# Performance work log

Hardware: AMD Instinct MI355X
Metric: run time of the kernel (lower is better)

## Reference

```python
import jax, jax.numpy as jnp
import numpy as np

# Model dims
T, B, J, H, K, N_LAYERS = 512, 64, 256, 256, 25, 3
THETA = 1.0        # spike threshold
SIGMA_INIT = 0.5   # Dcls gaussian sigma (frozen, requires_grad=False)
EPS = 1e-5         # batchnorm eps
ALPHA = 5.0        # ATan surrogate alpha


@jax.custom_vjp
def atan_spike(v):
    # Heaviside forward, ATan surrogate backward (spikingjelly ATan, alpha=5)
    return (v > 0.0).astype(v.dtype)

def _atan_fwd(v):
    return atan_spike(v), v

def _atan_bwd(v, g):
    return (g * (ALPHA / 2.0) / (1.0 + (jnp.pi / 2.0 * ALPHA * v) ** 2),)

atan_spike.defvjp(_atan_fwd, _atan_bwd)


def gauss_kernel(W, P, sig):
    # Dcls1d version='gauss', kernel_count=1: gaussian-interpolated dense kernel.
    # W, P: (O, Jin) -> kernel (O, Jin, K)
    pos = jnp.arange(K, dtype=W.dtype)                  # dilated kernel positions
    c = P + K // 2                                      # shift P into [0, K)
    s = jnp.abs(sig) + 0.27                             # DCLS sigma floor
    g = jnp.exp(-0.5 * ((pos[None, None, :] - c[..., None]) / s) ** 2)
    g = g / (jnp.sum(g, axis=-1, keepdims=True) + 1e-7)  # normalize over positions
    return W[..., None] * g


def delay_lif_layer(x, W, P, beta, gamma, bb, U0):
    # x: (T, B, Jin) -> (T, B, O)
    kern = gauss_kernel(W, P, SIGMA_INIT)               # (O, Jin, K)
    xc = jnp.transpose(x, (1, 2, 0))                    # (B, Jin, T)
    y = jax.lax.conv_general_dilated(
        xc, kern, window_strides=(1,), padding=[(K - 1, 0)],  # causal left-pad
        dimension_numbers=('NCH', 'OIH', 'NCH'))        # (B, O, T)
    y = jnp.transpose(y, (2, 0, 1))                     # (T, B, O)
    # BatchNorm1d over the flattened (T*B) dim, per channel (training stats)
    mu = jnp.mean(y, axis=(0, 1))
    var = jnp.var(y, axis=(0, 1))
    y = (y - mu) * jax.lax.rsqrt(var + EPS) * gamma + bb

    # Soft-reset LIF recurrence over time (note: original passes RAW beta,
    # not sigmoid(beta), to the cell -- reproduced faithfully here).
    def step(carry, xt):
        Ut, St = carry
        Ut = beta * (Ut - THETA * St) + (1.0 - beta) * xt
        St = atan_spike(Ut - THETA)
        return (Ut, St), St

    _, o = jax.lax.scan(step, (U0, jnp.zeros_like(U0)), y)
    return o


def setup_inputs():
    key = jax.random.key(0)
    ks = jax.random.split(key, 5)
    # sparse binary spike input, [T, B, J]
    x = (jax.random.uniform(ks[0], (T, B, J)) < 0.2).astype(jnp.float32)
    bound = float(np.sqrt(6.0 / J))  # kaiming_uniform, relu gain, fan_in = J*1
    W = jax.random.uniform(ks[1], (N_LAYERS, H, J), minval=-bound, maxval=bound, dtype=jnp.float32)
    P = jax.random.uniform(ks[2], (N_LAYERS, H, J), minval=-(K // 2), maxval=K // 2, dtype=jnp.float32)
    beta = jax.random.uniform(ks[3], (N_LAYERS, H), minval=0.7, maxval=0.9, dtype=jnp.float32)
    gamma = jnp.ones((N_LAYERS, H), jnp.float32)
    bb = jnp.zeros((N_LAYERS, H), jnp.float32)
    U0 = jax.random.uniform(ks[4], (N_LAYERS, B, H), dtype=jnp.float32)  # RandomBatchwiseInit(0,1)
    return {"x": x, "W": W, "P": P, "beta": beta, "gamma": gamma, "bb": bb, "U0": U0}


def reference(x, W, P, beta, gamma, bb, U0):
    o = x
    for l in range(N_LAYERS):  # fixed small layer loop
        o = delay_lif_layer(o, W[l], P[l], beta[l], gamma[l], bb[l], U0[l])
    return o
```

## Files before the change

### kernel.cpp

```cpp
#include <hip/hip_runtime.h>
#include <math.h>

#define T_DIM 512
#define B_DIM 64
#define J_DIM 256
#define H_DIM 256
#define K_TAP 25
#define NL    3
#define M_DIM (T_DIM*B_DIM)
#define NBH   (B_DIM*H_DIM)
#define GUARD_ROWS 1536
#define GUARD_BYTES (GUARD_ROWS*J_DIM)

#define MB 128
#define NB 64
#define NST (K_TAP*(J_DIM/64))
#define BSET 20480

typedef __attribute__((ext_vector_type(4))) int   i32x4;

__device__ __forceinline__ void gl16(const void* g, void* l){
  __builtin_amdgcn_global_load_lds((const __attribute__((address_space(1))) unsigned int*)g,
                                   (__attribute__((address_space(3))) unsigned int*)l, 16, 0, 0);
}

__global__ void zero_guard_k(unsigned char* __restrict__ g, unsigned char* __restrict__ p){
  const int bid = blockIdx.x;
  if(bid < 96) *(uint4*)(g + (size_t)(bid*256 + threadIdx.x)*16) = (uint4){0,0,0,0};
  else         *(uint4*)(p + (size_t)((bid-96)*256 + threadIdx.x)*16) = (uint4){0,0,0,0};
}

__global__ void cast_u8_k(const float* __restrict__ x, unsigned char* __restrict__ s){
  const int i = blockIdx.x*256 + threadIdx.x;
  const float4 v = *(const float4*)(x + (size_t)i*4);
  uchar4 o; o.x=(unsigned char)v.x; o.y=(unsigned char)v.y;
  o.z=(unsigned char)v.z; o.w=(unsigned char)v.w;
  *(uchar4*)(s + (size_t)i*4) = o;
}

__global__ void build_kern_k(const float* __restrict__ W, const float* __restrict__ P,
                             signed char* __restrict__ k0, signed char* __restrict__ k1,
                             signed char* __restrict__ k2, float* __restrict__ fsc, int layer){
  __shared__ float red[256];
  const int o = blockIdx.x, j = threadIdx.x;
  const float w = W[(layer*H_DIM + o)*J_DIM + j];
  const float p = P[(layer*H_DIM + o)*J_DIM + j];
  const float c = p + 12.0f;
  const float sg = 0.77f;
  float v[K_TAP]; float ssum = 0.f;
#pragma unroll
  for(int k=0;k<K_TAP;k++){ float z = ((float)k - c)/sg; v[k] = expf(-0.5f*z*z); ssum += v[k]; }
  const float inv = 1.0f/(ssum + 1e-7f);
  float mv = 0.f;
#pragma unroll
  for(int k=0;k<K_TAP;k++){ v[k] = w * (v[k]*inv); mv = fmaxf(mv, fabsf(v[k])); }
  red[j] = mv; __syncthreads();
  for(int st=128; st; st>>=1){ if(j<st) red[j] = fmaxf(red[j], red[j+st]); __syncthreads(); }
  int e; frexpf(red[0], &e);
  const float invq = ldexpf(1.f, 22 - e);
#pragma unroll
  for(int k=0;k<K_TAP;k++){
    const int d = (K_TAP-1)-k;
    int q = (int)lrintf(v[k]*invq);
    const int b0 = (int)(signed char)(q & 0xFF); q = (q - b0) >> 8;
    const int b1 = (int)(signed char)(q & 0xFF); q = (q - b1) >> 8;
    const size_t idx = (size_t)(d*H_DIM + o)*J_DIM + j;
    k0[idx] = (signed char)b0; k1[idx] = (signed char)b1; k2[idx] = (signed char)q;
  }
  if(j==0) fsc[o] = ldexpf(1.f, e - 22);
}

__global__ __launch_bounds__(256,2) void conv_mfma_k(const unsigned char* __restrict__ spk,
    const signed char* __restrict__ k0, const signed char* __restrict__ k1,
    const signed char* __restrict__ k2, const float* __restrict__ fsc,
    float* __restrict__ y, long long* __restrict__ part){
  __shared__ unsigned char lds[3][BSET];
  const int tid = threadIdx.x, lane = tid & 63, wave = tid >> 6;
  const int bid = blockIdx.x;
  const int q   = (bid & 7)*128 + (bid >> 3);
  const int m0  = (q & 255) * MB;
  const int n0  = (q >> 8) * NB;
  const int wm0 = (wave >> 1) << 6;
  const int wn0 = (wave & 1) << 5;

  const int srow  = tid >> 2;
  const int sslot = ((tid & 3) ^ (srow >> 1)) & 3;
  const int rslot = ((((lane>>4) ^ (lane>>1)) & 3) << 4);

  i32x4 acc0[4][2], acc1[4][2], acc2[4][2];
#pragma unroll
  for(int m=0;m<4;m++)
#pragma unroll
    for(int n=0;n<2;n++){
      acc0[m][n] = (i32x4){0,0,0,0};
      acc1[m][n] = (i32x4){0,0,0,0};
      acc2[m][n] = (i32x4){0,0,0,0};
    }

#define STAGE(base,t) do{ \
    const int d_ = (t)>>2, jc_ = ((t)&3)<<6; \
    unsigned char* lb_ = (base); \
    const unsigned char* as_ = spk + (size_t)(m0 + srow - (d_<<6) + GUARD_ROWS)*J_DIM + jc_ + sslot*16; \
    gl16(as_,                    lb_        + wave*1024); \
    gl16(as_ + (size_t)64*J_DIM, lb_ + 4096 + wave*1024); \
    const size_t bo_ = (size_t)(d_*H_DIM + n0 + srow)*J_DIM + jc_ + sslot*16; \
    gl16(k0 + bo_, lb_ + 8192  + wave*1024); \
    gl16(k1 + bo_, lb_ + 12288 + wave*1024); \
    gl16(k2 + bo_, lb_ + 16384 + wave*1024); \
  }while(0)

  unsigned char* const L = &lds[0][0];

  STAGE(L, 0);
  STAGE(L + BSET, 1);

  int rb = 0;
  for(int t=0; t<NST; ++t){
    if(t < NST-1) asm volatile("s_waitcnt vmcnt(5)" ::: "memory");
    else          asm volatile("s_waitcnt vmcnt(0)" ::: "memory");
    __builtin_amdgcn_s_barrier();
    __builtin_amdgcn_sched_barrier(0);
    unsigned char* Lb = L + rb*BSET;
    i32x4 af[4], b0f[2], b1f[2], b2f[2];
#pragma unroll
    for(int m=0;m<4;m++)
      af[m] = *(const i32x4*)(Lb + (wm0 + m*16 + (lane&15))*64 + rslot);
#pragma unroll
    for(int n=0;n<2;n++){
      const int ro = (wn0 + n*16 + (lane&15))*64 + rslot;
      b0f[n] = *(const i32x4*)(Lb + 8192  + ro);
      b1f[n] = *(const i32x4*)(Lb + 12288 + ro);
      b2f[n] = *(const i32x4*)(Lb + 16384 + ro);
    }
    if(t+2 < NST){
      int sb = rb + 2; if(sb >= 3) sb -= 3;
      STAGE(L + sb*BSET, t+2);
    }
    __builtin_amdgcn_s_setprio(1);
#pragma unroll
    for(int m=0;m<4;m++)
#pragma unroll
      for(int n=0;n<2;n++){
        acc0[m][n] = __builtin_amdgcn_mfma_i32_16x16x64_i8(af[m], b0f[n], acc0[m][n], 0,0,0);
        acc1[m][n] = __builtin_amdgcn_mfma_i32_16x16x64_i8(af[m], b1f[n], acc1[m][n], 0,0,0);
        acc2[m][n] = __builtin_amdgcn_mfma_i32_16x16x64_i8(af[m], b2f[n], acc2[m][n], 0,0,0);
      }
    __builtin_amdgcn_s_setprio(0);
    rb += 1; if(rb == 3) rb = 0;
  }

  const int r0 = m0 + wm0 + ((lane>>4)<<2);
  const int c0 = n0 + wn0 + (lane&15);
  const double f0 = (double)fsc[c0];
  const double f1 = (double)fsc[c0+16];
#pragma unroll
  for(int n=0;n<2;n++){
    const double fs = n ? f1 : f0;
    long long s1 = 0; unsigned long long shi = 0, slo = 0;
#pragma unroll
    for(int m=0;m<4;m++)
#pragma unroll
      for(int r=0;r<4;r++){
        const long long cmb = ((long long)acc2[m][n][r] << 16)
                            + ((long long)acc1[m][n][r] << 8)
                            +  (long long)acc0[m][n][r];
        y[(size_t)(r0 + m*16 + r)*H_DIM + c0 + n*16] = (float)((double)cmb * fs);
        s1 += cmb;
        const __int128 sq = (__int128)cmb * cmb;
        slo += (unsigned long long)(unsigned int)sq;
        shi += (unsigned long long)(sq >> 32);
      }
    s1  += __shfl_xor(s1, 16);  s1  += __shfl_xor(s1, 32);
    shi += __shfl_xor(shi, 16); shi += __shfl_xor(shi, 32);
    slo += __shfl_xor(slo, 16); slo += __shfl_xor(slo, 32);
    if(lane < 16){
      const int c = c0 + n*16;
      atomicAdd((unsigned long long*)&part[c],       (unsigned long long)s1);
      atomicAdd((unsigned long long*)&part[256 + c], shi);
      atomicAdd((unsigned long long*)&part[512 + c], slo);
    }
  }
#undef STAGE
}

__global__ void bn_final_k(long long* __restrict__ part, const float* __restrict__ fsc,
                           float* __restrict__ sc, float* __restrict__ sh,
                           const float* __restrict__ gamma_, const float* __restrict__ bb_,
                           int layer){
  const int o = threadIdx.x;
  const long long s1           = part[o];
  const unsigned long long shi = (unsigned long long)part[256 + o];
  const unsigned long long slo = (unsigned long long)part[512 + o];
  part[o] = 0; part[256 + o] = 0; part[512 + o] = 0;
  const double fs  = (double)fsc[o];
  const double sy  = (double)s1 * fs;
  const double sy2 = ((double)shi * 4294967296.0 + (double)slo) * fs * fs;
  const double inv_n = 1.0 / (double)M_DIM;
  const double m   = sy * inv_n;
  const double var = sy2 * inv_n - m*m;
  const double rs  = 1.0 / sqrt(var + (double)1e-5f);
  const float g  = gamma_[layer*H_DIM + o];
  const float bv = bb_[layer*H_DIM + o];
  const float scale = (float)((double)g * rs);
  sc[o] = scale;
  sh[o] = (float)((double)bv - m*(double)scale);
}

template<typename TOUT>
__global__ void lif_k(const float* yin, TOUT* sout,
                      const float* __restrict__ sc_, const float* __restrict__ sh_,
                      const float* __restrict__ beta_, const float* __restrict__ U0_,
                      int layer){
  const int idx = blockIdx.x*64 + threadIdx.x;
  const int h = idx & (H_DIM-1);
  const float scale = sc_[h];
  const float shift = sh_[h];
  const float beta  = beta_[layer*H_DIM + h];
  const float ombeta = 1.0f - beta;
  float U = U0_[layer*NBH + idx];
  float S = 0.f;
  float cur[16];
#pragma unroll
  for(int i=0;i<16;i++) cur[i] = yin[(size_t)i*NBH + idx];
  for(int t=0;t<T_DIM;t+=16){
    float nx[16];
#pragma unroll
    for(int i=0;i<16;i++){
      const int tt = t + 16 + i;
      nx[i] = (tt < T_DIM) ? yin[(size_t)tt*NBH + idx] : 0.f;
    }
#pragma unroll
    for(int i=0;i<16;i++){
      const float yv = fmaf(cur[i], scale, shift);
      U = beta*(U - S) + ombeta*yv;
      S = (U > 1.0f) ? 1.f : 0.f;
      sout[(size_t)(t+i)*NBH + idx] = (TOUT)S;
    }
#pragma unroll
    for(int i=0;i<16;i++) cur[i] = nx[i];
  }
}

extern "C" void kernel_launch(void* const* d_in, const int* in_sizes, int n_in,
                              void* d_out, int out_size, void* d_ws, size_t ws_size,
                              hipStream_t stream){
  const float* x    = (const float*)d_in[0];
  const float* W    = (const float*)d_in[1];
  const float* P    = (const float*)d_in[2];
  const float* beta = (const float*)d_in[3];
  const float* gam  = (const float*)d_in[4];
  const float* bb   = (const float*)d_in[5];
  const float* U0   = (const float*)d_in[6];
  float* out = (float*)d_out;

  char* ws = (char*)d_ws;
  unsigned char* spk  = (unsigned char*)ws;
  unsigned char* spkd = spk + GUARD_BYTES;
  signed char*   k0   = (signed char*)(ws + 8781824);
  signed char*   k1   = (signed char*)(ws + 10420224);
  signed char*   k2   = (signed char*)(ws + 12058624);
  float*         fsc  = (float*)(ws + 13697024);
  long long*     part = (long long*)(ws + 13698048);
  float*         sc   = (float*)(ws + 13706240);
  float*         sh   = sc + 256;

  zero_guard_k<<<dim3(98), dim3(256), 0, stream>>>(spk, (unsigned char*)part);
  cast_u8_k<<<dim3((M_DIM*J_DIM)/1024), dim3(256), 0, stream>>>(x, spkd);

  for(int l=0;l<NL;l++){
    build_kern_k<<<dim3(H_DIM), dim3(J_DIM), 0, stream>>>(W, P, k0, k1, k2, fsc, l);
    conv_mfma_k<<<dim3((M_DIM/MB)*(H_DIM/NB)), dim3(256), 0, stream>>>(spk, k0, k1, k2, fsc, out, part);
    bn_final_k<<<dim3(1), dim3(H_DIM), 0, stream>>>(part, fsc, sc, sh, gam, bb, l);
    if(l < NL-1) lif_k<unsigned char><<<dim3(NBH/64), dim3(64), 0, stream>>>(out, spkd, sc, sh, beta, U0, l);
    else         lif_k<float>        <<<dim3(NBH/64), dim3(64), 0, stream>>>(out, out, sc, sh, beta, U0, l);
  }
}
```

Measured before the change: 544.0 us.

## Split A/B LDS staging with shallower A prefetch to fit three blocks per CU

Splits the shared-memory staging into a double-buffered spike (A) tile and a triple-buffered kernel-weight (B) tile. The A tile is prefetched only one step ahead while B stays two steps ahead, and the vmcnt wait thresholds are adjusted to match. LDS drops from 60KB to 52KB per block, and launch bounds go from 2 to 3 blocks per CU to raise occupancy. The cost is a shorter latency-hiding window for the A loads and tighter register limits, which could cause spills given the 24 accumulator vectors.

```diff
diff --git a/kernel.cpp b/kernel.cpp
--- a/kernel.cpp
+++ b/kernel.cpp
@@ -15,7 +15,7 @@
 #define MB 128
 #define NB 64
 #define NST (K_TAP*(J_DIM/64))
-#define BSET 20480
+#define BSETB 12288
 
 typedef __attribute__((ext_vector_type(4))) int   i32x4;
 
@@ -70,11 +70,12 @@
   if(j==0) fsc[o] = ldexpf(1.f, e - 22);
 }
 
-__global__ __launch_bounds__(256,2) void conv_mfma_k(const unsigned char* __restrict__ spk,
+__global__ __launch_bounds__(256,3) void conv_mfma_k(const unsigned char* __restrict__ spk,
     const signed char* __restrict__ k0, const signed char* __restrict__ k1,
     const signed char* __restrict__ k2, const float* __restrict__ fsc,
     float* __restrict__ y, long long* __restrict__ part){
-  __shared__ unsigned char lds[3][BSET];
+  __shared__ unsigned char ldsA[2][8192];
+  __shared__ unsigned char ldsB[3][BSETB];
   const int tid = threadIdx.x, lane = tid & 63, wave = tid >> 6;
   const int bid = blockIdx.x;
   const int q   = (bid & 7)*128 + (bid >> 3);
@@ -97,44 +98,54 @@
       acc2[m][n] = (i32x4){0,0,0,0};
     }
 
-#define STAGE(base,t) do{ \
+#define STAGE_A(buf,t) do{ \
     const int d_ = (t)>>2, jc_ = ((t)&3)<<6; \
-    unsigned char* lb_ = (base); \
+    unsigned char* lb_ = &ldsA[(buf)][0]; \
     const unsigned char* as_ = spk + (size_t)(m0 + srow - (d_<<6) + GUARD_ROWS)*J_DIM + jc_ + sslot*16; \
     gl16(as_,                    lb_        + wave*1024); \
     gl16(as_ + (size_t)64*J_DIM, lb_ + 4096 + wave*1024); \
+  }while(0)
+
+#define STAGE_B(sb,t) do{ \
+    const int d_ = (t)>>2, jc_ = ((t)&3)<<6; \
+    unsigned char* lb_ = &ldsB[(sb)][0]; \
     const size_t bo_ = (size_t)(d_*H_DIM + n0 + srow)*J_DIM + jc_ + sslot*16; \
-    gl16(k0 + bo_, lb_ + 8192  + wave*1024); \
-    gl16(k1 + bo_, lb_ + 12288 + wave*1024); \
-    gl16(k2 + bo_, lb_ + 16384 + wave*1024); \
+    gl16(k0 + bo_, lb_        + wave*1024); \
+    gl16(k1 + bo_, lb_ + 4096 + wave*1024); \
+    gl16(k2 + bo_, lb_ + 8192 + wave*1024); \
   }while(0)
 
-  unsigned char* const L = &lds[0][0];
-
-  STAGE(L, 0);
-  STAGE(L + BSET, 1);
+  STAGE_A(0, 0);
+  __builtin_amdgcn_sched_barrier(0);
+  STAGE_B(0, 0);
+  __builtin_amdgcn_sched_barrier(0);
+  STAGE_B(1, 1);
 
   int rb = 0;
   for(int t=0; t<NST; ++t){
-    if(t < NST-1) asm volatile("s_waitcnt vmcnt(5)" ::: "memory");
+    const int ab = t & 1;
+    if(t < NST-1) asm volatile("s_waitcnt vmcnt(3)" ::: "memory");
     else          asm volatile("s_waitcnt vmcnt(0)" ::: "memory");
     __builtin_amdgcn_s_barrier();
     __builtin_amdgcn_sched_barrier(0);
-    unsigned char* Lb = L + rb*BSET;
+    const unsigned char* La = &ldsA[ab][0];
+    const unsigned char* Lb = &ldsB[rb][0];
     i32x4 af[4], b0f[2], b1f[2], b2f[2];
 #pragma unroll
     for(int m=0;m<4;m++)
-      af[m] = *(const i32x4*)(Lb + (wm0 + m*16 + (lane&15))*64 + rslot);
+      af[m] = *(const i32x4*)(La + (wm0 + m*16 + (lane&15))*64 + rslot);
 #pragma unroll
     for(int n=0;n<2;n++){
       const int ro = (wn0 + n*16 + (lane&15))*64 + rslot;
-      b0f[n] = *(const i32x4*)(Lb + 8192  + ro);
-      b1f[n] = *(const i32x4*)(Lb + 12288 + ro);
-      b2f[n] = *(const i32x4*)(Lb + 16384 + ro);
-    }
+      b0f[n] = *(const i32x4*)(Lb + ro);
+      b1f[n] = *(const i32x4*)(Lb + 4096 + ro);
+      b2f[n] = *(const i32x4*)(Lb + 8192 + ro);
+    }
+    if(t+1 < NST) STAGE_A(ab^1, t+1);
+    __builtin_amdgcn_sched_barrier(0);
     if(t+2 < NST){
       int sb = rb + 2; if(sb >= 3) sb -= 3;
-      STAGE(L + sb*BSET, t+2);
+      STAGE_B(sb, t+2);
     }
     __builtin_amdgcn_s_setprio(1);
 #pragma unroll
@@ -180,7 +191,8 @@
       atomicAdd((unsigned long long*)&part[512 + c], slo);
     }
   }
-#undef STAGE
+#undef STAGE_A
+#undef STAGE_B
 }
 
 __global__ void bn_final_k(long long* __restrict__ part, const float* __restrict__ fsc,
```

After: 565.4 us. +3.9%, slower.

## Double-buffer 128-wide K chunks instead of triple-buffered 64-wide stages in conv MFMA

Applied to the files above, without the earlier changes.

The int8 MFMA conv GEMM main loop now stages 128-byte K slices (two 64-wide MFMA sub-steps per stage) into two 40 KB LDS buffers, replacing three 20 KB buffers holding 64-byte slices. This halves the number of barrier/waitcnt iterations and changes the LDS XOR swizzle to 8 slots per 128-byte row. In exchange the pipeline depth drops to one stage ahead with a full vmcnt(0) wait, and LDS use rises from 60 KB to 80 KB per block, which may reduce occupancy under launch_bounds(256,2).

```diff
diff --git a/kernel.cpp b/kernel.cpp
--- a/kernel.cpp
+++ b/kernel.cpp
@@ -14,8 +14,8 @@
 
 #define MB 128
 #define NB 64
-#define NST (K_TAP*(J_DIM/64))
-#define BSET 20480
+#define NPER 50
+#define SETB 40960
 
 typedef __attribute__((ext_vector_type(4))) int   i32x4;
 
@@ -74,7 +74,7 @@
     const signed char* __restrict__ k0, const signed char* __restrict__ k1,
     const signed char* __restrict__ k2, const float* __restrict__ fsc,
     float* __restrict__ y, long long* __restrict__ part){
-  __shared__ unsigned char lds[3][BSET];
+  __shared__ unsigned char lds[2][SETB];
   const int tid = threadIdx.x, lane = tid & 63, wave = tid >> 6;
   const int bid = blockIdx.x;
   const int q   = (bid & 7)*128 + (bid >> 3);
@@ -83,9 +83,10 @@
   const int wm0 = (wave >> 1) << 6;
   const int wn0 = (wave & 1) << 5;
 
-  const int srow  = tid >> 2;
-  const int sslot = ((tid & 3) ^ (srow >> 1)) & 3;
-  const int rslot = ((((lane>>4) ^ (lane>>1)) & 3) << 4);
+  const int srow32 = tid >> 3;
+  const int lcol   = (((tid & 7) ^ (srow32 & 7)) << 4);
+  const int wv1k   = wave * 1024;
+  const int l15 = lane & 15, l7 = lane & 7, lg = lane >> 4;
 
   i32x4 acc0[4][2], acc1[4][2], acc2[4][2];
 #pragma unroll
@@ -97,56 +98,56 @@
       acc2[m][n] = (i32x4){0,0,0,0};
     }
 
-#define STAGE(base,t) do{ \
-    const int d_ = (t)>>2, jc_ = ((t)&3)<<6; \
-    unsigned char* lb_ = (base); \
-    const unsigned char* as_ = spk + (size_t)(m0 + srow - (d_<<6) + GUARD_ROWS)*J_DIM + jc_ + sslot*16; \
-    gl16(as_,                    lb_        + wave*1024); \
-    gl16(as_ + (size_t)64*J_DIM, lb_ + 4096 + wave*1024); \
-    const size_t bo_ = (size_t)(d_*H_DIM + n0 + srow)*J_DIM + jc_ + sslot*16; \
-    gl16(k0 + bo_, lb_ + 8192  + wave*1024); \
-    gl16(k1 + bo_, lb_ + 12288 + wave*1024); \
-    gl16(k2 + bo_, lb_ + 16384 + wave*1024); \
+#define STAGE(sbase,p) do{ \
+    const int d_ = (p)>>1, jc_ = ((p)&1)<<7; \
+    unsigned char* lb_ = (sbase); \
+    const unsigned char* as_ = spk + (size_t)(m0 + srow32 - (d_<<6) + GUARD_ROWS)*J_DIM + jc_ + lcol; \
+    gl16(as_,                     lb_         + wv1k); \
+    gl16(as_ + (size_t)32*J_DIM,  lb_ + 4096  + wv1k); \
+    gl16(as_ + (size_t)64*J_DIM,  lb_ + 8192  + wv1k); \
+    gl16(as_ + (size_t)96*J_DIM,  lb_ + 12288 + wv1k); \
+    const size_t bo_ = (size_t)(d_*H_DIM + n0 + srow32)*J_DIM + jc_ + lcol; \
+    gl16(k0 + bo_,                    lb_ + 16384        + wv1k); \
+    gl16(k0 + bo_ + (size_t)32*J_DIM, lb_ + 16384 + 4096 + wv1k); \
+    gl16(k1 + bo_,                    lb_ + 24576        + wv1k); \
+    gl16(k1 + bo_ + (size_t)32*J_DIM, lb_ + 24576 + 4096 + wv1k); \
+    gl16(k2 + bo_,                    lb_ + 32768        + wv1k); \
+    gl16(k2 + bo_ + (size_t)32*J_DIM, lb_ + 32768 + 4096 + wv1k); \
   }while(0)
 
-  unsigned char* const L = &lds[0][0];
-
-  STAGE(L, 0);
-  STAGE(L + BSET, 1);
-
-  int rb = 0;
-  for(int t=0; t<NST; ++t){
-    if(t < NST-1) asm volatile("s_waitcnt vmcnt(5)" ::: "memory");
-    else          asm volatile("s_waitcnt vmcnt(0)" ::: "memory");
+  STAGE(&lds[0][0], 0);
+
+  for(int p=0; p<NPER; ++p){
+    asm volatile("s_waitcnt vmcnt(0)" ::: "memory");
     __builtin_amdgcn_s_barrier();
     __builtin_amdgcn_sched_barrier(0);
-    unsigned char* Lb = L + rb*BSET;
-    i32x4 af[4], b0f[2], b1f[2], b2f[2];
-#pragma unroll
-    for(int m=0;m<4;m++)
-      af[m] = *(const i32x4*)(Lb + (wm0 + m*16 + (lane&15))*64 + rslot);
-#pragma unroll
-    for(int n=0;n<2;n++){
-      const int ro = (wn0 + n*16 + (lane&15))*64 + rslot;
-      b0f[n] = *(const i32x4*)(Lb + 8192  + ro);
-      b1f[n] = *(const i32x4*)(Lb + 12288 + ro);
-      b2f[n] = *(const i32x4*)(Lb + 16384 + ro);
-    }
-    if(t+2 < NST){
-      int sb = rb + 2; if(sb >= 3) sb -= 3;
-      STAGE(L + sb*BSET, t+2);
-    }
-    __builtin_amdgcn_s_setprio(1);
-#pragma unroll
-    for(int m=0;m<4;m++)
+    if(p+1 < NPER) STAGE(&lds[(p+1)&1][0], p+1);
+    const unsigned char* S = &lds[p&1][0];
+#pragma unroll
+    for(int s=0;s<2;s++){
+      const int rs = (((lg + (s<<2)) ^ l7) << 4);
+      i32x4 af[4], b0f[2], b1f[2], b2f[2];
+#pragma unroll
+      for(int m=0;m<4;m++)
+        af[m] = *(const i32x4*)(S + (wm0 + m*16 + l15)*128 + rs);
 #pragma unroll
       for(int n=0;n<2;n++){
-        acc0[m][n] = __builtin_amdgcn_mfma_i32_16x16x64_i8(af[m], b0f[n], acc0[m][n], 0,0,0);
-        acc1[m][n] = __builtin_amdgcn_mfma_i32_16x16x64_i8(af[m], b1f[n], acc1[m][n], 0,0,0);
-        acc2[m][n] = __builtin_amdgcn_mfma_i32_16x16x64_i8(af[m], b2f[n], acc2[m][n], 0,0,0);
+        const int ro = (wn0 + n*16 + l15)*128 + rs;
+        b0f[n] = *(const i32x4*)(S + 16384 + ro);
+        b1f[n] = *(const i32x4*)(S + 24576 + ro);
+        b2f[n] = *(const i32x4*)(S + 32768 + ro);
       }
-    __builtin_amdgcn_s_setprio(0);
-    rb += 1; if(rb == 3) rb = 0;
+      __builtin_amdgcn_s_setprio(1);
+#pragma unroll
+      for(int m=0;m<4;m++)
+#pragma unroll
+        for(int n=0;n<2;n++){
+          acc0[m][n] = __builtin_amdgcn_mfma_i32_16x16x64_i8(af[m], b0f[n], acc0[m][n], 0,0,0);
+          acc1[m][n] = __builtin_amdgcn_mfma_i32_16x16x64_i8(af[m], b1f[n], acc1[m][n], 0,0,0);
+          acc2[m][n] = __builtin_amdgcn_mfma_i32_16x16x64_i8(af[m], b2f[n], acc2[m][n], 0,0,0);
+        }
+      __builtin_amdgcn_s_setprio(0);
+    }
   }
 
   const int r0 = m0 + wm0 + ((lane>>4)<<2);
```

Measured after the change: 479.2 us, median of 2. 11.9% less time.
